# Kernel tuning notes

Hardware: AMD Instinct MI355X
Metric: run time of the kernel (lower is better)

The kernel has to match this reference:

```python
import jax, jax.numpy as jnp
import numpy as np

B, S, H = 2, 2048, 1024
E, K, F = 64, 8, 512
NORM_TOPK = True
CAP_FACTOR = 2.0


def setup_inputs() -> dict:
    key = jax.random.key(0)
    k0, k1, k2, k3, k4 = jax.random.split(key, 5)
    s_h = 1.0 / np.sqrt(H)
    s_f = 1.0 / np.sqrt(F)
    return {
        "hidden_states": jax.random.normal(k0, (B, S, H), jnp.float32),
        "w_gate": jax.random.normal(k1, (H, E), jnp.float32) * s_h,  # gate: Linear(H->E), no bias
        "w1": jax.random.normal(k2, (E, H, F), jnp.float32) * s_h,   # gate_proj per expert
        "w3": jax.random.normal(k3, (E, H, F), jnp.float32) * s_h,   # up_proj per expert
        "w2": jax.random.normal(k4, (E, F, H), jnp.float32) * s_f,   # down_proj per expert
    }


def reference(hidden_states, w_gate, w1, w3, w2):
    b, s, h = hidden_states.shape
    e = w_gate.shape[1]
    t = b * s
    x = hidden_states.reshape(t, h)
    router_logits = x @ w_gate                                   # [T, E]
    probs = jax.nn.softmax(router_logits.astype(jnp.float32), axis=-1)
    topw, sel = jax.lax.top_k(probs, K)                          # [T, K]
    if NORM_TOPK:
        topw = topw / jnp.sum(topw, axis=-1, keepdims=True)
    topw = topw.astype(x.dtype)

    a = t * K                                                    # total assignments
    c = int(CAP_FACTOR * a / e)                                  # static per-expert capacity
    sel_flat = sel.reshape(a)
    w_flat = topw.reshape(a)
    tok = jnp.repeat(jnp.arange(t), K)
    order = jnp.argsort(sel_flat, stable=True)                   # group assignments by expert
    e_s, t_s, w_s = sel_flat[order], tok[order], w_flat[order]
    counts = jnp.bincount(sel_flat, length=e)
    starts = jnp.cumsum(counts) - counts
    pos = jnp.arange(a) - starts[e_s]                            # position within expert group
    valid = pos < c
    slot = jnp.where(valid, e_s * c + pos, e * c)                # overflow -> dropped sentinel slot

    # dispatch: gather tokens into per-expert contiguous buffer [E, C, H]
    buf = jnp.zeros((e * c + 1, h), x.dtype).at[slot].set(x[t_s])
    xb = buf[: e * c].reshape(e, c, h)
    # grouped gated-SiLU MLP per expert
    g = jnp.einsum('ech,ehf->ecf', xb, w1)
    u = jnp.einsum('ech,ehf->ecf', xb, w3)
    yb = jnp.einsum('ecf,efh->ech', jax.nn.silu(g) * u, w2).reshape(e * c, h)
    # combine: weighted scatter-add back to tokens
    contrib = yb[jnp.minimum(slot, e * c - 1)] * (w_s * valid.astype(x.dtype))[:, None]
    out = jnp.zeros((t, h), x.dtype).at[t_s].add(contrib)
    return out.reshape(b, s, h), router_logits
```

## Files before the change

kernel.cpp:

```cpp
#include <hip/hip_runtime.h>
#include <hip/hip_bf16.h>

#define T_TOK 4096
#define H_DIM 1024
#define E_EXP 64
#define TOPK  8
#define F_DIM 512
#define CAP   1024
#define A_TOT (T_TOK * TOPK)

typedef _Float16 f16;
typedef _Float16 f16x8 __attribute__((ext_vector_type(8)));
typedef float    f32x4 __attribute__((ext_vector_type(4)));

__global__ __launch_bounds__(256) void pack_w_kernel(
    const float* __restrict__ src, f16* __restrict__ dst, int Kd, int Nd)
{
    const int tid  = threadIdx.x;
    const int lane = tid & 63, wv = tid >> 6;
    const int kbs = __builtin_ctz(Kd >> 5);
    const int nts = __builtin_ctz(Nd >> 4);
    const int chunk = blockIdx.x * 4 + wv;
    const int kt = chunk & ((1 << kbs) - 1);
    const int en = chunk >> kbs;
    const int nt = en & ((1 << nts) - 1);
    const int e  = en >> nts;
    const int jj = lane & 15, qq = lane >> 4;
    const float* s = src + ((size_t)e * Kd + kt * 32 + qq * 8) * Nd + nt * 16 + jj;
    f16x8 v;
    #pragma unroll
    for (int j = 0; j < 8; ++j) v[j] = (f16)s[(size_t)j * Nd];
    *(f16x8*)(dst + (size_t)chunk * 512 + lane * 8) = v;
}

__global__ __launch_bounds__(256) void router_kernel(
    const float* __restrict__ x, const float* __restrict__ wg,
    float* __restrict__ logits_out, int* __restrict__ sel,
    float* __restrict__ wgtA, f16* __restrict__ xh)
{
    __shared__ float xs[16][128];
    __shared__ float ls[16][65];
    const int tid = threadIdx.x;
    const int e  = tid & 63;
    const int tg = tid >> 6;
    const int tb = blockIdx.x * 16;

    float acc[4] = {0.f, 0.f, 0.f, 0.f};
    for (int h0 = 0; h0 < H_DIM; h0 += 128) {
        {
            int r  = tid >> 4;
            int c0 = (tid & 15) * 8;
            const float4* src = (const float4*)(x + (size_t)(tb + r) * H_DIM + h0 + c0);
            float4 v0 = src[0], v1 = src[1];
            *(float4*)&xs[r][c0]     = v0;
            *(float4*)&xs[r][c0 + 4] = v1;
            f16x8 hv;
            hv[0] = (f16)v0.x; hv[1] = (f16)v0.y; hv[2] = (f16)v0.z; hv[3] = (f16)v0.w;
            hv[4] = (f16)v1.x; hv[5] = (f16)v1.y; hv[6] = (f16)v1.z; hv[7] = (f16)v1.w;
            *(f16x8*)(xh + (size_t)(tb + r) * H_DIM + h0 + c0) = hv;
        }
        __syncthreads();
        for (int hh = 0; hh < 128; ++hh) {
            float w = wg[(size_t)(h0 + hh) * E_EXP + e];
            #pragma unroll
            for (int i = 0; i < 4; ++i)
                acc[i] = fmaf(xs[tg * 4 + i][hh], w, acc[i]);
        }
        __syncthreads();
    }
    #pragma unroll
    for (int i = 0; i < 4; ++i) {
        int tt = tg * 4 + i;
        logits_out[(size_t)(tb + tt) * E_EXP + e] = acc[i];
        ls[tt][e] = acc[i];
    }
    __syncthreads();
    if (tid < 16) {
        int tt = tid;
        float lv[8]; int li[8];
        for (int k = 0; k < 8; ++k) {
            float m = -1e30f; int mi = 0;
            for (int j = 0; j < 64; ++j) {
                float v = ls[tt][j];
                if (v > m) { m = v; mi = j; }
            }
            lv[k] = m; li[k] = mi;
            ls[tt][mi] = -1e30f;
        }
        float s = 0.f, wv[8];
        for (int k = 0; k < 8; ++k) { wv[k] = __expf(lv[k] - lv[0]); s += wv[k]; }
        float inv = 1.f / s;
        for (int k = 0; k < 8; ++k) {
            int a = (tb + tt) * TOPK + k;
            sel[a]  = li[k];
            wgtA[a] = wv[k] * inv;
        }
    }
}

__global__ __launch_bounds__(256) void build_lists_kernel(
    const int* __restrict__ sel,
    int* __restrict__ tok_list, int* __restrict__ slotA,
    int* __restrict__ counts)
{
    __shared__ int sc[256];
    const int e = blockIdx.x;
    const int tid = threadIdx.x;
    const int per = A_TOT / 256;
    const int a0 = tid * per;
    int cnt = 0;
    for (int i = 0; i < per; ++i) cnt += (sel[a0 + i] == e) ? 1 : 0;
    sc[tid] = cnt;
    __syncthreads();
    for (int s = 1; s < 256; s <<= 1) {
        int v = (tid >= s) ? sc[tid - s] : 0;
        __syncthreads();
        sc[tid] += v;
        __syncthreads();
    }
    int total = sc[255];
    int pos = sc[tid] - cnt;
    if (tid == 0) counts[e] = (total < CAP) ? total : CAP;
    for (int i = 0; i < per; ++i) {
        int a = a0 + i;
        if (sel[a] == e) {
            if (pos < CAP) {
                tok_list[e * CAP + pos] = a >> 3;
                slotA[a] = e * CAP + pos;
            } else {
                slotA[a] = -1;
            }
            pos++;
        }
    }
}

#define MFMA16(a, b, c) __builtin_amdgcn_mfma_f32_16x16x32_f16(a, b, c, 0, 0, 0)

__global__ __launch_bounds__(256) void gemm1_kernel(
    const f16* __restrict__ xh, const f16* __restrict__ w1p,
    const f16* __restrict__ w3p, const int* __restrict__ tok_list,
    const int* __restrict__ counts, f16* __restrict__ P)
{
    const int id = blockIdx.x;
    const int x7 = id & 7, r = id >> 3;
    const int ft = r & 7, mt = (r >> 3) & 15, eh = r >> 7;
    const int e = x7 + 8 * eh;
    const int cnt = counts[e];
    const int m0 = mt * 64;
    if (m0 >= cnt) return;
    const int bf = ft * 64;

    __shared__ f16 Xs[2][64][72];
    __shared__ int tok_s[64];

    const int tid = threadIdx.x;
    const int lane = tid & 63, wv = tid >> 6;
    const int jj = lane & 15, qq = lane >> 4;
    const int sr = tid >> 3, sc = (tid & 7) * 8;

    if (tid < 64) {
        int m = m0 + tid;
        tok_s[tid] = (m < cnt) ? tok_list[e * CAP + m] : tok_list[e * CAP];
    }
    __syncthreads();
    const size_t rowA = (size_t)tok_s[sr] * H_DIM + sc;
    const size_t rowB = (size_t)tok_s[sr + 32] * H_DIM + sc;

    const f16* w1b = w1p + (((size_t)e * 32 + ft * 4 + wv) * 32) * 512 + lane * 8;
    const f16* w3b = w3p + (((size_t)e * 32 + ft * 4 + wv) * 32) * 512 + lane * 8;

    f32x4 accG[4], accU[4];
    #pragma unroll
    for (int i = 0; i < 4; ++i) {
        accG[i] = (f32x4){0.f, 0.f, 0.f, 0.f};
        accU[i] = (f32x4){0.f, 0.f, 0.f, 0.f};
    }

    {
        f16x8 a = *(const f16x8*)(xh + rowA);
        f16x8 b = *(const f16x8*)(xh + rowB);
        *(f16x8*)&Xs[0][sr][sc]      = a;
        *(f16x8*)&Xs[0][sr + 32][sc] = b;
    }
    f16x8 cG0 = *(const f16x8*)(w1b);
    f16x8 cG1 = *(const f16x8*)(w1b + 512);
    f16x8 cU0 = *(const f16x8*)(w3b);
    f16x8 cU1 = *(const f16x8*)(w3b + 512);

    #pragma unroll
    for (int it = 0; it < 16; ++it) {
        const int k0 = it * 64;
        __syncthreads();
        f16x8 xn0, xn1, nG0, nG1, nU0, nU1;
        if (it < 15) {
            xn0 = *(const f16x8*)(xh + rowA + k0 + 64);
            xn1 = *(const f16x8*)(xh + rowB + k0 + 64);
            size_t kg = (size_t)(2 * it + 2) * 512;
            nG0 = *(const f16x8*)(w1b + kg);
            nG1 = *(const f16x8*)(w1b + kg + 512);
            nU0 = *(const f16x8*)(w3b + kg);
            nU1 = *(const f16x8*)(w3b + kg + 512);
        }
        const int buf = it & 1;
        #pragma unroll
        for (int m2 = 0; m2 < 4; ++m2) {
            f16x8 a0 = *(const f16x8*)&Xs[buf][m2 * 16 + jj][qq * 8];
            f16x8 a1 = *(const f16x8*)&Xs[buf][m2 * 16 + jj][32 + qq * 8];
            accG[m2] = MFMA16(a0, cG0, accG[m2]);
            accU[m2] = MFMA16(a0, cU0, accU[m2]);
            accG[m2] = MFMA16(a1, cG1, accG[m2]);
            accU[m2] = MFMA16(a1, cU1, accU[m2]);
        }
        if (it < 15) {
            *(f16x8*)&Xs[buf ^ 1][sr][sc]      = xn0;
            *(f16x8*)&Xs[buf ^ 1][sr + 32][sc] = xn1;
            cG0 = nG0; cG1 = nG1; cU0 = nU0; cU1 = nU1;
        }
    }
    #pragma unroll
    for (int m2 = 0; m2 < 4; ++m2) {
        #pragma unroll
        for (int rr = 0; rr < 4; ++rr) {
            int row = m2 * 16 + qq * 4 + rr;
            float gg = accG[m2][rr], u = accU[m2][rr];
            float p = gg / (1.f + __expf(-gg)) * u;
            P[(size_t)(e * CAP + m0 + row) * F_DIM + bf + wv * 16 + jj] = (f16)p;
        }
    }
}

__global__ __launch_bounds__(256) void gemm2_kernel(
    const f16* __restrict__ P, const f16* __restrict__ w2p,
    const int* __restrict__ counts, f16* __restrict__ Y)
{
    const int id = blockIdx.x;
    const int x7 = id & 7, r = id >> 3;
    const int ht = r & 7, mt = (r >> 3) & 15, eh = r >> 7;
    const int e = x7 + 8 * eh;
    const int cnt = counts[e];
    const int m0 = mt * 64;
    if (m0 >= cnt) return;
    const int h0 = ht * 128;

    __shared__ f16 Ps[2][64][72];

    const int tid = threadIdx.x;
    const int lane = tid & 63, wv = tid >> 6;
    const int jj = lane & 15, qq = lane >> 4;
    const int sr = tid >> 3, sc = (tid & 7) * 8;

    const size_t pbase = (size_t)(e * CAP + m0) * F_DIM;
    const f16* wA = w2p + (((size_t)e * 64 + ht * 8 + wv) * 16) * 512 + lane * 8;
    const f16* wB = w2p + (((size_t)e * 64 + ht * 8 + wv + 4) * 16) * 512 + lane * 8;

    f32x4 accA[4], accB[4];
    #pragma unroll
    for (int i = 0; i < 4; ++i) {
        accA[i] = (f32x4){0.f, 0.f, 0.f, 0.f};
        accB[i] = (f32x4){0.f, 0.f, 0.f, 0.f};
    }

    {
        f16x8 a = *(const f16x8*)(P + pbase + (size_t)sr * F_DIM + sc);
        f16x8 b = *(const f16x8*)(P + pbase + (size_t)(sr + 32) * F_DIM + sc);
        *(f16x8*)&Ps[0][sr][sc]      = a;
        *(f16x8*)&Ps[0][sr + 32][sc] = b;
    }
    f16x8 cA0 = *(const f16x8*)(wA);
    f16x8 cA1 = *(const f16x8*)(wA + 512);
    f16x8 cB0 = *(const f16x8*)(wB);
    f16x8 cB1 = *(const f16x8*)(wB + 512);

    #pragma unroll
    for (int it = 0; it < 8; ++it) {
        const int k0 = it * 64;
        __syncthreads();
        f16x8 pn0, pn1, nA0, nA1, nB0, nB1;
        if (it < 7) {
            pn0 = *(const f16x8*)(P + pbase + (size_t)sr * F_DIM + k0 + 64 + sc);
            pn1 = *(const f16x8*)(P + pbase + (size_t)(sr + 32) * F_DIM + k0 + 64 + sc);
            size_t kg = (size_t)(2 * it + 2) * 512;
            nA0 = *(const f16x8*)(wA + kg);
            nA1 = *(const f16x8*)(wA + kg + 512);
            nB0 = *(const f16x8*)(wB + kg);
            nB1 = *(const f16x8*)(wB + kg + 512);
        }
        const int buf = it & 1;
        #pragma unroll
        for (int m2 = 0; m2 < 4; ++m2) {
            f16x8 a0 = *(const f16x8*)&Ps[buf][m2 * 16 + jj][qq * 8];
            f16x8 a1 = *(const f16x8*)&Ps[buf][m2 * 16 + jj][32 + qq * 8];
            accA[m2] = MFMA16(a0, cA0, accA[m2]);
            accB[m2] = MFMA16(a0, cB0, accB[m2]);
            accA[m2] = MFMA16(a1, cA1, accA[m2]);
            accB[m2] = MFMA16(a1, cB1, accB[m2]);
        }
        if (it < 7) {
            *(f16x8*)&Ps[buf ^ 1][sr][sc]      = pn0;
            *(f16x8*)&Ps[buf ^ 1][sr + 32][sc] = pn1;
            cA0 = nA0; cA1 = nA1; cB0 = nB0; cB1 = nB1;
        }
    }
    f16* yb = Y + (size_t)(e * CAP + m0) * H_DIM + h0 + wv * 16 + jj;
    #pragma unroll
    for (int m2 = 0; m2 < 4; ++m2) {
        #pragma unroll
        for (int rr = 0; rr < 4; ++rr) {
            int row = m2 * 16 + qq * 4 + rr;
            yb[(size_t)row * H_DIM]      = (f16)accA[m2][rr];
            yb[(size_t)row * H_DIM + 64] = (f16)accB[m2][rr];
        }
    }
}

__global__ __launch_bounds__(256) void combine_kernel(
    const f16* __restrict__ Y, const int* __restrict__ slotA,
    const float* __restrict__ wgtA, float* __restrict__ out)
{
    const int tid = threadIdx.x;
    const int t  = blockIdx.x * 2 + (tid >> 7);
    const int hc = (tid & 127) * 8;
    float acc[8] = {0.f, 0.f, 0.f, 0.f, 0.f, 0.f, 0.f, 0.f};
    const int base = t * TOPK;
    #pragma unroll
    for (int k = 0; k < 8; ++k) {
        int s   = slotA[base + k];
        float w = wgtA[base + k];
        if (s >= 0) {
            f16x8 y = *(const f16x8*)(Y + (size_t)s * H_DIM + hc);
            #pragma unroll
            for (int j = 0; j < 8; ++j) acc[j] += w * (float)y[j];
        }
    }
    float4 o0 = {acc[0], acc[1], acc[2], acc[3]};
    float4 o1 = {acc[4], acc[5], acc[6], acc[7]};
    *(float4*)(out + (size_t)t * H_DIM + hc)     = o0;
    *(float4*)(out + (size_t)t * H_DIM + hc + 4) = o1;
}

extern "C" void kernel_launch(void* const* d_in, const int* in_sizes, int n_in,
                              void* d_out, int out_size, void* d_ws, size_t ws_size,
                              hipStream_t stream) {
    const float* x  = (const float*)d_in[0];
    const float* wg = (const float*)d_in[1];
    const float* w1 = (const float*)d_in[2];
    const float* w3 = (const float*)d_in[3];
    const float* w2 = (const float*)d_in[4];

    float* out    = (float*)d_out;
    float* logits = out + (size_t)T_TOK * H_DIM;

    char* ws = (char*)d_ws;
    int*   sel      = (int*)  (ws);
    float* wgtA     = (float*)(ws + (128 << 10));
    int*   tok_list = (int*)  (ws + (256 << 10));
    int*   slotA    = (int*)  (ws + (512 << 10));
    int*   counts   = (int*)  (ws + (768 << 10));
    f16*   xh       = (f16*)  (ws + (size_t)(1 << 20));
    f16*   P        = (f16*)  (ws + (size_t)(9 << 20));
    f16*   w1p      = (f16*)  (ws + (size_t)(73 << 20));
    f16*   w3p      = (f16*)  (ws + (size_t)(137 << 20));
    f16*   w2p      = (f16*)  (ws + (size_t)(201 << 20));
    f16*   Y        = (f16*)  (ws + (size_t)(73 << 20));

    pack_w_kernel<<<16384, 256, 0, stream>>>(w1, w1p, H_DIM, F_DIM);
    pack_w_kernel<<<16384, 256, 0, stream>>>(w3, w3p, H_DIM, F_DIM);
    pack_w_kernel<<<16384, 256, 0, stream>>>(w2, w2p, F_DIM, H_DIM);
    router_kernel<<<T_TOK / 16, 256, 0, stream>>>(x, wg, logits, sel, wgtA, xh);
    build_lists_kernel<<<E_EXP, 256, 0, stream>>>(sel, tok_list, slotA, counts);
    gemm1_kernel<<<8192, 256, 0, stream>>>(xh, w1p, w3p, tok_list, counts, P);
    gemm2_kernel<<<8192, 256, 0, stream>>>(P, w2p, counts, Y);
    combine_kernel<<<T_TOK / 2, 256, 0, stream>>>(Y, slotA, wgtA, out);
}
```

Baseline: 661.2 us.

## Widen expert GEMM N-tiles and swizzle LDS instead of padding

Both grouped GEMMs now give each block twice the output columns: gemm1 covers 128 F columns and gemm2 covers 256 H columns. Each wave computes more MFMA N-subtiles per A fragment loaded from LDS, and the grid is halved. This is meant to cut redundant gathers of token rows and P rows and to reduce LDS traffic per MFMA. The padded LDS tiles are replaced by an XOR-swizzled 64-wide layout to avoid bank conflicts without padding. In exchange, register pressure rises (more accumulators and prefetched weight fragments), which may lower occupancy, and there are fewer blocks to spread across CUs.

```diff
diff --git a/kernel.cpp b/kernel.cpp
--- a/kernel.cpp
+++ b/kernel.cpp
@@ -144,20 +144,24 @@
 {
     const int id = blockIdx.x;
     const int x7 = id & 7, r = id >> 3;
-    const int ft = r & 7, mt = (r >> 3) & 15, eh = r >> 7;
+    const int ft = r & 3, mt = (r >> 2) & 15, eh = r >> 6;
     const int e = x7 + 8 * eh;
     const int cnt = counts[e];
     const int m0 = mt * 64;
     if (m0 >= cnt) return;
-    const int bf = ft * 64;
-
-    __shared__ f16 Xs[2][64][72];
+    const int bf = ft * 128;
+
+    __shared__ f16 Xs[2][64][64];
     __shared__ int tok_s[64];
 
     const int tid = threadIdx.x;
     const int lane = tid & 63, wv = tid >> 6;
     const int jj = lane & 15, qq = lane >> 4;
     const int sr = tid >> 3, sc = (tid & 7) * 8;
+    const int swz_w = ((tid & 7) ^ (sr & 7)) * 8;
+    const int x8 = jj & 7;
+    const int s0 = (qq ^ x8) * 8;
+    const int s1 = ((qq + 4) ^ x8) * 8;
 
     if (tid < 64) {
         int m = m0 + tid;
@@ -167,65 +171,85 @@
     const size_t rowA = (size_t)tok_s[sr] * H_DIM + sc;
     const size_t rowB = (size_t)tok_s[sr + 32] * H_DIM + sc;
 
-    const f16* w1b = w1p + (((size_t)e * 32 + ft * 4 + wv) * 32) * 512 + lane * 8;
-    const f16* w3b = w3p + (((size_t)e * 32 + ft * 4 + wv) * 32) * 512 + lane * 8;
-
-    f32x4 accG[4], accU[4];
-    #pragma unroll
-    for (int i = 0; i < 4; ++i) {
-        accG[i] = (f32x4){0.f, 0.f, 0.f, 0.f};
-        accU[i] = (f32x4){0.f, 0.f, 0.f, 0.f};
-    }
+    const int ntA = ft * 8 + wv * 2;
+    const f16* w1a = w1p + ((size_t)(e * 32 + ntA) * 32) * 512 + lane * 8;
+    const f16* w3a = w3p + ((size_t)(e * 32 + ntA) * 32) * 512 + lane * 8;
+
+    f32x4 accG[4][2], accU[4][2];
+    #pragma unroll
+    for (int i = 0; i < 4; ++i)
+        #pragma unroll
+        for (int n = 0; n < 2; ++n) {
+            accG[i][n] = (f32x4){0.f, 0.f, 0.f, 0.f};
+            accU[i][n] = (f32x4){0.f, 0.f, 0.f, 0.f};
+        }
 
     {
         f16x8 a = *(const f16x8*)(xh + rowA);
         f16x8 b = *(const f16x8*)(xh + rowB);
-        *(f16x8*)&Xs[0][sr][sc]      = a;
-        *(f16x8*)&Xs[0][sr + 32][sc] = b;
-    }
-    f16x8 cG0 = *(const f16x8*)(w1b);
-    f16x8 cG1 = *(const f16x8*)(w1b + 512);
-    f16x8 cU0 = *(const f16x8*)(w3b);
-    f16x8 cU1 = *(const f16x8*)(w3b + 512);
+        *(f16x8*)&Xs[0][sr][swz_w]      = a;
+        *(f16x8*)&Xs[0][sr + 32][swz_w] = b;
+    }
+    f16x8 cG[4], cU[4];
+    cG[0] = *(const f16x8*)(w1a);
+    cG[1] = *(const f16x8*)(w1a + 512);
+    cG[2] = *(const f16x8*)(w1a + 16384);
+    cG[3] = *(const f16x8*)(w1a + 16384 + 512);
+    cU[0] = *(const f16x8*)(w3a);
+    cU[1] = *(const f16x8*)(w3a + 512);
+    cU[2] = *(const f16x8*)(w3a + 16384);
+    cU[3] = *(const f16x8*)(w3a + 16384 + 512);
 
     #pragma unroll
     for (int it = 0; it < 16; ++it) {
         const int k0 = it * 64;
         __syncthreads();
-        f16x8 xn0, xn1, nG0, nG1, nU0, nU1;
+        f16x8 xn0, xn1, nG[4], nU[4];
         if (it < 15) {
             xn0 = *(const f16x8*)(xh + rowA + k0 + 64);
             xn1 = *(const f16x8*)(xh + rowB + k0 + 64);
             size_t kg = (size_t)(2 * it + 2) * 512;
-            nG0 = *(const f16x8*)(w1b + kg);
-            nG1 = *(const f16x8*)(w1b + kg + 512);
-            nU0 = *(const f16x8*)(w3b + kg);
-            nU1 = *(const f16x8*)(w3b + kg + 512);
+            nG[0] = *(const f16x8*)(w1a + kg);
+            nG[1] = *(const f16x8*)(w1a + kg + 512);
+            nG[2] = *(const f16x8*)(w1a + kg + 16384);
+            nG[3] = *(const f16x8*)(w1a + kg + 16384 + 512);
+            nU[0] = *(const f16x8*)(w3a + kg);
+            nU[1] = *(const f16x8*)(w3a + kg + 512);
+            nU[2] = *(const f16x8*)(w3a + kg + 16384);
+            nU[3] = *(const f16x8*)(w3a + kg + 16384 + 512);
         }
         const int buf = it & 1;
         #pragma unroll
         for (int m2 = 0; m2 < 4; ++m2) {
-            f16x8 a0 = *(const f16x8*)&Xs[buf][m2 * 16 + jj][qq * 8];
-            f16x8 a1 = *(const f16x8*)&Xs[buf][m2 * 16 + jj][32 + qq * 8];
-            accG[m2] = MFMA16(a0, cG0, accG[m2]);
-            accU[m2] = MFMA16(a0, cU0, accU[m2]);
-            accG[m2] = MFMA16(a1, cG1, accG[m2]);
-            accU[m2] = MFMA16(a1, cU1, accU[m2]);
+            f16x8 a0 = *(const f16x8*)&Xs[buf][m2 * 16 + jj][s0];
+            f16x8 a1 = *(const f16x8*)&Xs[buf][m2 * 16 + jj][s1];
+            accG[m2][0] = MFMA16(a0, cG[0], accG[m2][0]);
+            accG[m2][0] = MFMA16(a1, cG[1], accG[m2][0]);
+            accG[m2][1] = MFMA16(a0, cG[2], accG[m2][1]);
+            accG[m2][1] = MFMA16(a1, cG[3], accG[m2][1]);
+            accU[m2][0] = MFMA16(a0, cU[0], accU[m2][0]);
+            accU[m2][0] = MFMA16(a1, cU[1], accU[m2][0]);
+            accU[m2][1] = MFMA16(a0, cU[2], accU[m2][1]);
+            accU[m2][1] = MFMA16(a1, cU[3], accU[m2][1]);
         }
         if (it < 15) {
-            *(f16x8*)&Xs[buf ^ 1][sr][sc]      = xn0;
-            *(f16x8*)&Xs[buf ^ 1][sr + 32][sc] = xn1;
-            cG0 = nG0; cG1 = nG1; cU0 = nU0; cU1 = nU1;
+            *(f16x8*)&Xs[buf ^ 1][sr][swz_w]      = xn0;
+            *(f16x8*)&Xs[buf ^ 1][sr + 32][swz_w] = xn1;
+            #pragma unroll
+            for (int i = 0; i < 4; ++i) { cG[i] = nG[i]; cU[i] = nU[i]; }
         }
     }
     #pragma unroll
     for (int m2 = 0; m2 < 4; ++m2) {
         #pragma unroll
-        for (int rr = 0; rr < 4; ++rr) {
-            int row = m2 * 16 + qq * 4 + rr;
-            float gg = accG[m2][rr], u = accU[m2][rr];
-            float p = gg / (1.f + __expf(-gg)) * u;
-            P[(size_t)(e * CAP + m0 + row) * F_DIM + bf + wv * 16 + jj] = (f16)p;
+        for (int n = 0; n < 2; ++n) {
+            #pragma unroll
+            for (int rr = 0; rr < 4; ++rr) {
+                int row = m2 * 16 + qq * 4 + rr;
+                float gg = accG[m2][n][rr], u = accU[m2][n][rr];
+                float p = gg / (1.f + __expf(-gg)) * u;
+                P[(size_t)(e * CAP + m0 + row) * F_DIM + bf + (wv * 2 + n) * 16 + jj] = (f16)p;
+            }
         }
     }
 }
@@ -236,80 +260,90 @@
 {
     const int id = blockIdx.x;
     const int x7 = id & 7, r = id >> 3;
-    const int ht = r & 7, mt = (r >> 3) & 15, eh = r >> 7;
+    const int ht = r & 3, mt = (r >> 2) & 15, eh = r >> 6;
     const int e = x7 + 8 * eh;
     const int cnt = counts[e];
     const int m0 = mt * 64;
     if (m0 >= cnt) return;
-    const int h0 = ht * 128;
-
-    __shared__ f16 Ps[2][64][72];
+    const int h0 = ht * 256;
+
+    __shared__ f16 Ps[2][64][64];
 
     const int tid = threadIdx.x;
     const int lane = tid & 63, wv = tid >> 6;
     const int jj = lane & 15, qq = lane >> 4;
     const int sr = tid >> 3, sc = (tid & 7) * 8;
+    const int swz_w = ((tid & 7) ^ (sr & 7)) * 8;
+    const int x8 = jj & 7;
+    const int s0 = (qq ^ x8) * 8;
+    const int s1 = ((qq + 4) ^ x8) * 8;
 
     const size_t pbase = (size_t)(e * CAP + m0) * F_DIM;
-    const f16* wA = w2p + (((size_t)e * 64 + ht * 8 + wv) * 16) * 512 + lane * 8;
-    const f16* wB = w2p + (((size_t)e * 64 + ht * 8 + wv + 4) * 16) * 512 + lane * 8;
-
-    f32x4 accA[4], accB[4];
-    #pragma unroll
-    for (int i = 0; i < 4; ++i) {
-        accA[i] = (f32x4){0.f, 0.f, 0.f, 0.f};
-        accB[i] = (f32x4){0.f, 0.f, 0.f, 0.f};
-    }
+    const int nt0 = ht * 16 + wv * 4;
+    const f16* wb = w2p + ((size_t)(e * 64 + nt0) * 16) * 512 + lane * 8;
+
+    f32x4 acc[4][4];
+    #pragma unroll
+    for (int i = 0; i < 4; ++i)
+        #pragma unroll
+        for (int n = 0; n < 4; ++n)
+            acc[i][n] = (f32x4){0.f, 0.f, 0.f, 0.f};
 
     {
         f16x8 a = *(const f16x8*)(P + pbase + (size_t)sr * F_DIM + sc);
         f16x8 b = *(const f16x8*)(P + pbase + (size_t)(sr + 32) * F_DIM + sc);
-        *(f16x8*)&Ps[0][sr][sc]      = a;
-        *(f16x8*)&Ps[0][sr + 32][sc] = b;
-    }
-    f16x8 cA0 = *(const f16x8*)(wA);
-    f16x8 cA1 = *(const f16x8*)(wA + 512);
-    f16x8 cB0 = *(const f16x8*)(wB);
-    f16x8 cB1 = *(const f16x8*)(wB + 512);
+        *(f16x8*)&Ps[0][sr][swz_w]      = a;
+        *(f16x8*)&Ps[0][sr + 32][swz_w] = b;
+    }
+    f16x8 cW[8];
+    #pragma unroll
+    for (int i = 0; i < 4; ++i) {
+        cW[i * 2]     = *(const f16x8*)(wb + (size_t)i * 8192);
+        cW[i * 2 + 1] = *(const f16x8*)(wb + (size_t)i * 8192 + 512);
+    }
 
     #pragma unroll
     for (int it = 0; it < 8; ++it) {
         const int k0 = it * 64;
         __syncthreads();
-        f16x8 pn0, pn1, nA0, nA1, nB0, nB1;
+        f16x8 pn0, pn1, nW[8];
         if (it < 7) {
             pn0 = *(const f16x8*)(P + pbase + (size_t)sr * F_DIM + k0 + 64 + sc);
             pn1 = *(const f16x8*)(P + pbase + (size_t)(sr + 32) * F_DIM + k0 + 64 + sc);
             size_t kg = (size_t)(2 * it + 2) * 512;
-            nA0 = *(const f16x8*)(wA + kg);
-            nA1 = *(const f16x8*)(wA + kg + 512);
-            nB0 = *(const f16x8*)(wB + kg);
-            nB1 = *(const f16x8*)(wB + kg + 512);
+            #pragma unroll
+            for (int i = 0; i < 4; ++i) {
+                nW[i * 2]     = *(const f16x8*)(wb + (size_t)i * 8192 + kg);
+                nW[i * 2 + 1] = *(const f16x8*)(wb + (size_t)i * 8192 + kg + 512);
+            }
         }
         const int buf = it & 1;
         #pragma unroll
         for (int m2 = 0; m2 < 4; ++m2) {
-            f16x8 a0 = *(const f16x8*)&Ps[buf][m2 * 16 + jj][qq * 8];
-            f16x8 a1 = *(const f16x8*)&Ps[buf][m2 * 16 + jj][32 + qq * 8];
-            accA[m2] = MFMA16(a0, cA0, accA[m2]);
-            accB[m2] = MFMA16(a0, cB0, accB[m2]);
-            accA[m2] = MFMA16(a1, cA1, accA[m2]);
-            accB[m2] = MFMA16(a1, cB1, accB[m2]);
+            f16x8 a0 = *(const f16x8*)&Ps[buf][m2 * 16 + jj][s0];
+            f16x8 a1 = *(const f16x8*)&Ps[buf][m2 * 16 + jj][s1];
+            #pragma unroll
+            for (int i = 0; i < 4; ++i) {
+                acc[m2][i] = MFMA16(a0, cW[i * 2],     acc[m2][i]);
+                acc[m2][i] = MFMA16(a1, cW[i * 2 + 1], acc[m2][i]);
+            }
         }
         if (it < 7) {
-            *(f16x8*)&Ps[buf ^ 1][sr][sc]      = pn0;
-            *(f16x8*)&Ps[buf ^ 1][sr + 32][sc] = pn1;
-            cA0 = nA0; cA1 = nA1; cB0 = nB0; cB1 = nB1;
-        }
-    }
-    f16* yb = Y + (size_t)(e * CAP + m0) * H_DIM + h0 + wv * 16 + jj;
+            *(f16x8*)&Ps[buf ^ 1][sr][swz_w]      = pn0;
+            *(f16x8*)&Ps[buf ^ 1][sr + 32][swz_w] = pn1;
+            #pragma unroll
+            for (int i = 0; i < 8; ++i) cW[i] = nW[i];
+        }
+    }
+    f16* yb = Y + (size_t)(e * CAP + m0) * H_DIM + h0 + wv * 64 + jj;
     #pragma unroll
     for (int m2 = 0; m2 < 4; ++m2) {
         #pragma unroll
         for (int rr = 0; rr < 4; ++rr) {
             int row = m2 * 16 + qq * 4 + rr;
-            yb[(size_t)row * H_DIM]      = (f16)accA[m2][rr];
-            yb[(size_t)row * H_DIM + 64] = (f16)accB[m2][rr];
+            #pragma unroll
+            for (int i = 0; i < 4; ++i)
+                yb[(size_t)row * H_DIM + i * 16] = (f16)acc[m2][i][rr];
         }
     }
 }
@@ -369,7 +403,7 @@
     pack_w_kernel<<<16384, 256, 0, stream>>>(w2, w2p, F_DIM, H_DIM);
     router_kernel<<<T_TOK / 16, 256, 0, stream>>>(x, wg, logits, sel, wgtA, xh);
     build_lists_kernel<<<E_EXP, 256, 0, stream>>>(sel, tok_list, slotA, counts);
-    gemm1_kernel<<<8192, 256, 0, stream>>>(xh, w1p, w3p, tok_list, counts, P);
-    gemm2_kernel<<<8192, 256, 0, stream>>>(P, w2p, counts, Y);
+    gemm1_kernel<<<4096, 256, 0, stream>>>(xh, w1p, w3p, tok_list, counts, P);
+    gemm2_kernel<<<4096, 256, 0, stream>>>(P, w2p, counts, Y);
     combine_kernel<<<T_TOK / 2, 256, 0, stream>>>(Y, slotA, wgtA, out);
 }
```

Measured after the change: 684.1 us. 3.5% more time.

## Merge weight packing into one kernel and XOR-swizzle GEMM LDS tiles

Applied to the files above, without the earlier changes.

The three weight-packing launches become a single kernel in which each wave converts two adjacent 16-column tiles, so each row read covers 32 contiguous floats instead of 16. In both expert GEMM kernels the padded 72-column LDS tiles are replaced by unpadded 64-column tiles whose 8-element chunks are XOR-swizzled by row, so MFMA operand reads avoid bank conflicts without the padding. The intent is fewer launches, better-coalesced packing reads, and less shared memory per block. The swizzle index math must stay consistent between the LDS writes and reads.

```diff
diff --git a/kernel.cpp b/kernel.cpp
--- a/kernel.cpp
+++ b/kernel.cpp
@@ -13,24 +13,36 @@
 typedef _Float16 f16x8 __attribute__((ext_vector_type(8)));
 typedef float    f32x4 __attribute__((ext_vector_type(4)));
 
-__global__ __launch_bounds__(256) void pack_w_kernel(
-    const float* __restrict__ src, f16* __restrict__ dst, int Kd, int Nd)
+__global__ __launch_bounds__(256) void pack_all_kernel(
+    const float* __restrict__ w1, const float* __restrict__ w3,
+    const float* __restrict__ w2,
+    f16* __restrict__ w1p, f16* __restrict__ w3p, f16* __restrict__ w2p)
 {
     const int tid  = threadIdx.x;
-    const int lane = tid & 63, wv = tid >> 6;
-    const int kbs = __builtin_ctz(Kd >> 5);
-    const int nts = __builtin_ctz(Nd >> 4);
-    const int chunk = blockIdx.x * 4 + wv;
-    const int kt = chunk & ((1 << kbs) - 1);
-    const int en = chunk >> kbs;
-    const int nt = en & ((1 << nts) - 1);
-    const int e  = en >> nts;
+    const int lane = tid & 63, wvi = tid >> 6;
+    int pid = blockIdx.x * 4 + wvi;
+    const float* src; f16* dst; int Nd, kb, kbs, nps;
+    if (pid < 32768)      { src = w1; dst = w1p; Nd = 512;  kb = 32; kbs = 5; nps = 4; }
+    else if (pid < 65536) { src = w3; dst = w3p; Nd = 512;  kb = 32; kbs = 5; nps = 4; pid -= 32768; }
+    else                  { src = w2; dst = w2p; Nd = 1024; kb = 16; kbs = 4; nps = 5; pid -= 65536; }
+    const int kt  = pid & (kb - 1);
+    const int en  = pid >> kbs;
+    const int ntp = en & ((1 << nps) - 1);
+    const int e   = en >> nps;
+    const int Kd  = kb << 5;
     const int jj = lane & 15, qq = lane >> 4;
-    const float* s = src + ((size_t)e * Kd + kt * 32 + qq * 8) * Nd + nt * 16 + jj;
-    f16x8 v;
-    #pragma unroll
-    for (int j = 0; j < 8; ++j) v[j] = (f16)s[(size_t)j * Nd];
-    *(f16x8*)(dst + (size_t)chunk * 512 + lane * 8) = v;
+    const float* s = src + ((size_t)e * Kd + kt * 32 + qq * 8) * Nd + ntp * 32 + jj;
+    f16x8 v0, v1;
+    #pragma unroll
+    for (int j = 0; j < 8; ++j) {
+        float a = s[(size_t)j * Nd];
+        float b = s[(size_t)j * Nd + 16];
+        v0[j] = (f16)a;
+        v1[j] = (f16)b;
+    }
+    size_t c0 = (size_t)(e * (Nd >> 4) + ntp * 2) * kb + kt;
+    *(f16x8*)(dst + c0 * 512 + lane * 8)        = v0;
+    *(f16x8*)(dst + (c0 + kb) * 512 + lane * 8) = v1;
 }
 
 __global__ __launch_bounds__(256) void router_kernel(
@@ -151,13 +163,17 @@
     if (m0 >= cnt) return;
     const int bf = ft * 64;
 
-    __shared__ f16 Xs[2][64][72];
+    __shared__ f16 Xs[2][64][64];
     __shared__ int tok_s[64];
 
     const int tid = threadIdx.x;
     const int lane = tid & 63, wv = tid >> 6;
     const int jj = lane & 15, qq = lane >> 4;
     const int sr = tid >> 3, sc = (tid & 7) * 8;
+    const int swz_w = ((tid & 7) ^ (sr & 7)) * 8;
+    const int x8 = jj & 7;
+    const int s0 = (qq ^ x8) * 8;
+    const int s1 = ((qq + 4) ^ x8) * 8;
 
     if (tid < 64) {
         int m = m0 + tid;
@@ -167,8 +183,9 @@
     const size_t rowA = (size_t)tok_s[sr] * H_DIM + sc;
     const size_t rowB = (size_t)tok_s[sr + 32] * H_DIM + sc;
 
-    const f16* w1b = w1p + (((size_t)e * 32 + ft * 4 + wv) * 32) * 512 + lane * 8;
-    const f16* w3b = w3p + (((size_t)e * 32 + ft * 4 + wv) * 32) * 512 + lane * 8;
+    const int nt = ft * 4 + wv;
+    const f16* w1a = w1p + ((size_t)(e * 32 + nt) * 32) * 512 + lane * 8;
+    const f16* w3a = w3p + ((size_t)(e * 32 + nt) * 32) * 512 + lane * 8;
 
     f32x4 accG[4], accU[4];
     #pragma unroll
@@ -180,13 +197,13 @@
     {
         f16x8 a = *(const f16x8*)(xh + rowA);
         f16x8 b = *(const f16x8*)(xh + rowB);
-        *(f16x8*)&Xs[0][sr][sc]      = a;
-        *(f16x8*)&Xs[0][sr + 32][sc] = b;
-    }
-    f16x8 cG0 = *(const f16x8*)(w1b);
-    f16x8 cG1 = *(const f16x8*)(w1b + 512);
-    f16x8 cU0 = *(const f16x8*)(w3b);
-    f16x8 cU1 = *(const f16x8*)(w3b + 512);
+        *(f16x8*)&Xs[0][sr][swz_w]      = a;
+        *(f16x8*)&Xs[0][sr + 32][swz_w] = b;
+    }
+    f16x8 cG0 = *(const f16x8*)(w1a);
+    f16x8 cG1 = *(const f16x8*)(w1a + 512);
+    f16x8 cU0 = *(const f16x8*)(w3a);
+    f16x8 cU1 = *(const f16x8*)(w3a + 512);
 
     #pragma unroll
     for (int it = 0; it < 16; ++it) {
@@ -197,24 +214,24 @@
             xn0 = *(const f16x8*)(xh + rowA + k0 + 64);
             xn1 = *(const f16x8*)(xh + rowB + k0 + 64);
             size_t kg = (size_t)(2 * it + 2) * 512;
-            nG0 = *(const f16x8*)(w1b + kg);
-            nG1 = *(const f16x8*)(w1b + kg + 512);
-            nU0 = *(const f16x8*)(w3b + kg);
-            nU1 = *(const f16x8*)(w3b + kg + 512);
+            nG0 = *(const f16x8*)(w1a + kg);
+            nG1 = *(const f16x8*)(w1a + kg + 512);
+            nU0 = *(const f16x8*)(w3a + kg);
+            nU1 = *(const f16x8*)(w3a + kg + 512);
         }
         const int buf = it & 1;
         #pragma unroll
         for (int m2 = 0; m2 < 4; ++m2) {
-            f16x8 a0 = *(const f16x8*)&Xs[buf][m2 * 16 + jj][qq * 8];
-            f16x8 a1 = *(const f16x8*)&Xs[buf][m2 * 16 + jj][32 + qq * 8];
+            f16x8 a0 = *(const f16x8*)&Xs[buf][m2 * 16 + jj][s0];
+            f16x8 a1 = *(const f16x8*)&Xs[buf][m2 * 16 + jj][s1];
             accG[m2] = MFMA16(a0, cG0, accG[m2]);
             accU[m2] = MFMA16(a0, cU0, accU[m2]);
             accG[m2] = MFMA16(a1, cG1, accG[m2]);
             accU[m2] = MFMA16(a1, cU1, accU[m2]);
         }
         if (it < 15) {
-            *(f16x8*)&Xs[buf ^ 1][sr][sc]      = xn0;
-            *(f16x8*)&Xs[buf ^ 1][sr + 32][sc] = xn1;
+            *(f16x8*)&Xs[buf ^ 1][sr][swz_w]      = xn0;
+            *(f16x8*)&Xs[buf ^ 1][sr + 32][swz_w] = xn1;
             cG0 = nG0; cG1 = nG1; cU0 = nU0; cU1 = nU1;
         }
     }
@@ -243,16 +260,20 @@
     if (m0 >= cnt) return;
     const int h0 = ht * 128;
 
-    __shared__ f16 Ps[2][64][72];
+    __shared__ f16 Ps[2][64][64];
 
     const int tid = threadIdx.x;
     const int lane = tid & 63, wv = tid >> 6;
     const int jj = lane & 15, qq = lane >> 4;
     const int sr = tid >> 3, sc = (tid & 7) * 8;
+    const int swz_w = ((tid & 7) ^ (sr & 7)) * 8;
+    const int x8 = jj & 7;
+    const int s0 = (qq ^ x8) * 8;
+    const int s1 = ((qq + 4) ^ x8) * 8;
 
     const size_t pbase = (size_t)(e * CAP + m0) * F_DIM;
-    const f16* wA = w2p + (((size_t)e * 64 + ht * 8 + wv) * 16) * 512 + lane * 8;
-    const f16* wB = w2p + (((size_t)e * 64 + ht * 8 + wv + 4) * 16) * 512 + lane * 8;
+    const f16* wA = w2p + ((size_t)(e * 64 + ht * 8 + wv) * 16) * 512 + lane * 8;
+    const f16* wB = w2p + ((size_t)(e * 64 + ht * 8 + wv + 4) * 16) * 512 + lane * 8;
 
     f32x4 accA[4], accB[4];
     #pragma unroll
@@ -264,8 +285,8 @@
     {
         f16x8 a = *(const f16x8*)(P + pbase + (size_t)sr * F_DIM + sc);
         f16x8 b = *(const f16x8*)(P + pbase + (size_t)(sr + 32) * F_DIM + sc);
-        *(f16x8*)&Ps[0][sr][sc]      = a;
-        *(f16x8*)&Ps[0][sr + 32][sc] = b;
+        *(f16x8*)&Ps[0][sr][swz_w]      = a;
+        *(f16x8*)&Ps[0][sr + 32][swz_w] = b;
     }
     f16x8 cA0 = *(const f16x8*)(wA);
     f16x8 cA1 = *(const f16x8*)(wA + 512);
@@ -289,16 +310,16 @@
         const int buf = it & 1;
         #pragma unroll
         for (int m2 = 0; m2 < 4; ++m2) {
-            f16x8 a0 = *(const f16x8*)&Ps[buf][m2 * 16 + jj][qq * 8];
-            f16x8 a1 = *(const f16x8*)&Ps[buf][m2 * 16 + jj][32 + qq * 8];
+            f16x8 a0 = *(const f16x8*)&Ps[buf][m2 * 16 + jj][s0];
+            f16x8 a1 = *(const f16x8*)&Ps[buf][m2 * 16 + jj][s1];
             accA[m2] = MFMA16(a0, cA0, accA[m2]);
             accB[m2] = MFMA16(a0, cB0, accB[m2]);
             accA[m2] = MFMA16(a1, cA1, accA[m2]);
             accB[m2] = MFMA16(a1, cB1, accB[m2]);
         }
         if (it < 7) {
-            *(f16x8*)&Ps[buf ^ 1][sr][sc]      = pn0;
-            *(f16x8*)&Ps[buf ^ 1][sr + 32][sc] = pn1;
+            *(f16x8*)&Ps[buf ^ 1][sr][swz_w]      = pn0;
+            *(f16x8*)&Ps[buf ^ 1][sr + 32][swz_w] = pn1;
             cA0 = nA0; cA1 = nA1; cB0 = nB0; cB1 = nB1;
         }
     }
@@ -364,9 +385,7 @@
     f16*   w2p      = (f16*)  (ws + (size_t)(201 << 20));
     f16*   Y        = (f16*)  (ws + (size_t)(73 << 20));
 
-    pack_w_kernel<<<16384, 256, 0, stream>>>(w1, w1p, H_DIM, F_DIM);
-    pack_w_kernel<<<16384, 256, 0, stream>>>(w3, w3p, H_DIM, F_DIM);
-    pack_w_kernel<<<16384, 256, 0, stream>>>(w2, w2p, F_DIM, H_DIM);
+    pack_all_kernel<<<24576, 256, 0, stream>>>(w1, w3, w2, w1p, w3p, w2p);
     router_kernel<<<T_TOK / 16, 256, 0, stream>>>(x, wg, logits, sel, wgtA, xh);
     build_lists_kernel<<<E_EXP, 256, 0, stream>>>(sel, tok_list, slotA, counts);
     gemm1_kernel<<<8192, 256, 0, stream>>>(xh, w1p, w3p, tok_list, counts, P);
```

Result: no change. 655.4 us (-0.9%).
